# Kernel tuning notes

Hardware: AMD Instinct MI355X
Metric: run time of the kernel (lower is better)

## Reference

```python
import jax, jax.numpy as jnp
import numpy as np

FEW, BATCH, D, STEPS = 128, 4096, 512, 4


def setup_inputs() -> dict:
    key = jax.random.key(0)
    ks = jax.random.split(key, 6)
    H = 2 * D  # LSTMCell hidden size
    return {
        "support": jax.random.normal(ks[0], (FEW, D), jnp.float32),
        "query": jax.random.normal(ks[1], (BATCH, D), jnp.float32),
        "W_ih": jax.random.normal(ks[2], (4 * H, D), jnp.float32) * (1.0 / np.sqrt(H)),
        "W_hh": jax.random.normal(ks[3], (4 * H, H), jnp.float32) * (1.0 / np.sqrt(H)),
        "b_ih": jax.random.normal(ks[4], (4 * H,), jnp.float32) * 0.01,
        "b_hh": jax.random.normal(ks[5], (4 * H,), jnp.float32) * 0.01,
        "process_step": STEPS,
    }


def reference(support, query, W_ih, W_hh, b_ih, b_hh, process_step):
    # support: (few, d); query: (batch, d); LSTMCell hidden = 2d.
    d = query.shape[1]
    batch = query.shape[0]
    h_r = jnp.zeros((batch, 2 * d), query.dtype)
    c = jnp.zeros((batch, 2 * d), query.dtype)
    h = query
    for _ in range(process_step):
        # PyTorch LSTMCell: gates ordered (i, f, g, o)
        gates = query @ W_ih.T + b_ih + h_r @ W_hh.T + b_hh  # (batch, 8d)
        i, f, g, o = jnp.split(gates, 4, axis=1)
        c = jax.nn.sigmoid(f) * c + jax.nn.sigmoid(i) * jnp.tanh(g)
        h_r_ = jax.nn.sigmoid(o) * jnp.tanh(c)  # (batch, 2d)
        h = query + h_r_[:, :d]  # (batch, d)
        attn = jax.nn.softmax(h @ support.T, axis=1)  # (batch, few)
        r = attn @ support  # (batch, d)
        h_r = jnp.concatenate([h, r], axis=1)  # (batch, 2d)
    return h
```

## Files before the change

### kernel.cpp

```cpp
#include <hip/hip_runtime.h>

#define BATCH 4096
#define DDIM  512
#define FEWN  128
#define LDA1  640
#define GATEN 2048
#define CDIM  512

typedef unsigned short ushort_t;
typedef __attribute__((ext_vector_type(8))) short bf16x8;
typedef __attribute__((ext_vector_type(4))) float f32x4;

__device__ inline ushort_t f2bf(float f) {
  unsigned u = __float_as_uint(f);
  unsigned r = (u + 0x7FFFu + ((u >> 16) & 1u)) >> 16;
  return (ushort_t)r;
}
__device__ inline float bf2f(ushort_t h) { return __uint_as_float((unsigned)h << 16); }
__device__ inline float bf2f_u(unsigned h16) { return __uint_as_float(h16 << 16); }

__device__ inline float sigmoidf(float x) { return 1.f / (1.f + __expf(-x)); }
__device__ inline float tanh_fast(float x) {
  float ax = fabsf(x);
  float t = __expf(-2.f * ax);
  float r = (1.f - t) / (1.f + t);
  return copysignf(r, x);
}

__device__ inline int orig_row(int colp) {
  return ((colp >> 4) & 3) * 1024 + ((colp >> 6) << 4) + (colp & 15);
}

__device__ inline void async_copy16(ushort_t* lds, const ushort_t* g) {
  __builtin_amdgcn_global_load_lds(
      (const __attribute__((address_space(1))) unsigned int*)g,
      (__attribute__((address_space(3))) unsigned int*)lds, 16, 0, 0);
}

#define XCD_SWZ()                                                            \
  int bx = blockIdx.x, by = blockIdx.y;                                      \
  {                                                                          \
    const int gx = gridDim.x;                                                \
    const int id = by * gx + bx;                                             \
    if ((gx & 7) == 0) {                                                     \
      const int cpx = gx >> 3;                                               \
      const int x = id & 7, s = id >> 3;                                     \
      bx = x * cpx + (s % cpx);                                              \
      by = s / cpx;                                                          \
    } else {                                                                 \
      const int nwg = gx * gridDim.y;                                        \
      const int qq = nwg >> 3, rr = nwg & 7;                                 \
      const int x = id & 7, s = id >> 3;                                     \
      const int nid = (x < rr ? x * (qq + 1) : rr * (qq + 1) + (x - rr) * qq) + s; \
      bx = nid % gx; by = nid / gx;                                          \
    }                                                                        \
  }

#define STAGE8(dA, dB, kk)                                                   \
    async_copy16(dA,              gA0 + (kk));                               \
    async_copy16(dA + 512,        gA0 + (size_t)16 * lda + (kk));            \
    async_copy16(dA + 4096,       gA0 + (kk) + 32);                          \
    async_copy16(dA + 4096 + 512, gA0 + (size_t)16 * lda + (kk) + 32);       \
    async_copy16(dB,              gB0 + (kk));                               \
    async_copy16(dB + 512,        gB0 + (size_t)16 * ldb + (kk));            \
    async_copy16(dB + 4096,       gB0 + (kk) + 32);                          \
    async_copy16(dB + 4096 + 512, gB0 + (size_t)16 * ldb + (kk) + 32);

#define KLOOP_DBUF()                                                         \
  const int nIter = K >> 6;                                                  \
  { STAGE8(sA, sB, 0) }                                                      \
  if (nIter > 1) { STAGE8(sA + 8192, sB + 8192, 64) }                        \
  for (int kt = 0; kt < nIter; ++kt) {                                       \
    if (kt + 1 < nIter) asm volatile("s_waitcnt vmcnt(8)" ::: "memory");     \
    else                asm volatile("s_waitcnt vmcnt(0)" ::: "memory");     \
    __builtin_amdgcn_s_barrier();                                            \
    const int cur = (kt & 1) * 8192;                                         \
    _Pragma("unroll")                                                        \
    for (int h = 0; h < 2; ++h) {                                            \
      bf16x8 af[4], bfr[4];                                                  \
      _Pragma("unroll")                                                      \
      for (int mi = 0; mi < 4; ++mi)                                         \
        af[mi] = *(const bf16x8*)&lA[cur + h * 4096 + (wr * 64 + mi * 16 + lr) * 32 + kg * 8]; \
      _Pragma("unroll")                                                      \
      for (int ni = 0; ni < 4; ++ni)                                         \
        bfr[ni] = *(const bf16x8*)&lB[cur + h * 4096 + (wc * 64 + ni * 16 + lr) * 32 + kg * 8]; \
      _Pragma("unroll")                                                      \
      for (int mi = 0; mi < 4; ++mi)                                         \
        _Pragma("unroll")                                                    \
        for (int ni = 0; ni < 4; ++ni)                                       \
          acc[mi][ni] = __builtin_amdgcn_mfma_f32_16x16x32_bf16(af[mi], bfr[ni], acc[mi][ni], 0, 0, 0); \
    }                                                                        \
    __builtin_amdgcn_s_barrier();                                            \
    if (kt + 2 < nIter) {                                                    \
      const int k2 = (kt + 2) << 6;                                          \
      STAGE8(sA + cur, sB + cur, k2)                                         \
    }                                                                        \
  }

#define GEMM_PROLOG()                                                        \
  __shared__ __align__(16) ushort_t lA[2 * 8192];                            \
  __shared__ __align__(16) ushort_t lB[2 * 8192];                            \
  const int tid = threadIdx.x;                                               \
  const int wid = tid >> 6, lane = tid & 63;                                 \
  const int wr = wid >> 1, wc = wid & 1;                                     \
  XCD_SWZ()                                                                  \
  const int m0 = by * 128, n0 = bx * 128;                                    \
  const int lr = lane & 15, kg = lane >> 4;                                  \
  f32x4 acc[4][4] = {};                                                      \
  const int srow = lane >> 2;                                                \
  const int scol = (lane & 3) * 8;                                           \
  const ushort_t* gA0 = A + (size_t)(m0 + wid * 32 + srow) * lda + scol;     \
  const ushort_t* gB0 = B + (size_t)(n0 + wid * 32 + srow) * ldb + scol;     \
  ushort_t* sA = &lA[wid * 1024];                                            \
  ushort_t* sB = &lB[wid * 1024];                                            \
  KLOOP_DBUF()

__launch_bounds__(256)
__global__ void gemm_wide(const ushort_t* __restrict__ A, const ushort_t* __restrict__ B,
                          ushort_t* __restrict__ gbase, ushort_t* __restrict__ c,
                          ushort_t* __restrict__ A1out, ushort_t* __restrict__ A2out,
                          const float* __restrict__ b1, const float* __restrict__ b2,
                          int K, int lda, int ldb) {
  GEMM_PROLOG()
  if (n0 < 2048) {
    const int jj = ((n0 + wc * 64) >> 6) * 16 + lr;
    const float bi0 = b1[jj]        + b2[jj];
    const float bi2 = b1[2048 + jj] + b2[2048 + jj];
    const float bi3 = b1[3072 + jj] + b2[3072 + jj];
#pragma unroll
    for (int mi = 0; mi < 4; ++mi) {
#pragma unroll
      for (int r = 0; r < 4; ++r) {
        const int row = m0 + wr * 64 + mi * 16 + kg * 4 + r;
        const float si = sigmoidf(acc[mi][0][r] + bi0);
        const float tg = tanh_fast(acc[mi][2][r] + bi2);
        const float so = sigmoidf(acc[mi][3][r] + bi3);
        const float cn = si * tg;
        c[(size_t)row * CDIM + jj] = f2bf(cn);
        const float hr = so * tanh_fast(cn);
        const ushort_t hi = f2bf(hr);
        const ushort_t lo = f2bf(hr - bf2f(hi));
        A1out[(size_t)row * LDA1 + jj] = hi;
        A2out[(size_t)row * DDIM + jj] = lo;
      }
    }
  } else {
    const int jj = ((n0 - 2048 + wc * 64) >> 6) * 16 + lr;
    const float bi0 = b1[jj]        + b2[jj];
    const float bi1 = b1[1024 + jj] + b2[1024 + jj];
    const float bi2 = b1[2048 + jj] + b2[2048 + jj];
    const float bi3 = b1[3072 + jj] + b2[3072 + jj];
#pragma unroll
    for (int mi = 0; mi < 4; ++mi)
#pragma unroll
      for (int r = 0; r < 4; ++r) {
        const int row = m0 + wr * 64 + mi * 16 + kg * 4 + r;
        uint2 p;
        p.x = (unsigned)f2bf(acc[mi][0][r] + bi0) | ((unsigned)f2bf(acc[mi][1][r] + bi1) << 16);
        p.y = (unsigned)f2bf(acc[mi][2][r] + bi2) | ((unsigned)f2bf(acc[mi][3][r] + bi3) << 16);
        *(uint2*)&gbase[(size_t)row * GATEN + jj * 4] = p;
      }
  }
}

template<int MODE>
__launch_bounds__(256)
__global__ void gemm_fused(const ushort_t* __restrict__ A, const ushort_t* __restrict__ B,
                           const ushort_t* __restrict__ base, ushort_t* __restrict__ c,
                           ushort_t* __restrict__ A1out, ushort_t* __restrict__ A2out,
                           const float* __restrict__ query, float* __restrict__ out,
                           int K, int lda, int ldb) {
  GEMM_PROLOG()
  const int jj = ((n0 + wc * 64) >> 6) * 16 + lr;
#pragma unroll
  for (int mi = 0; mi < 4; ++mi) {
#pragma unroll
    for (int r = 0; r < 4; ++r) {
      const int row = m0 + wr * 64 + mi * 16 + kg * 4 + r;
      const uint2 p = *(const uint2*)&base[(size_t)row * GATEN + jj * 4];
      const float g0 = bf2f_u(p.x & 0xFFFFu) + acc[mi][0][r];
      const float g1 = bf2f_u(p.x >> 16)     + acc[mi][1][r];
      const float g2 = bf2f_u(p.y & 0xFFFFu) + acc[mi][2][r];
      const float g3 = bf2f_u(p.y >> 16)     + acc[mi][3][r];
      const float si = sigmoidf(g0);
      const float sf = sigmoidf(g1);
      const float tg = tanh_fast(g2);
      const float so = sigmoidf(g3);
      const size_t ci = (size_t)row * CDIM + jj;
      const float cn = sf * bf2f(c[ci]) + si * tg;
      if (MODE != 2) c[ci] = f2bf(cn);
      const float hr = so * tanh_fast(cn);
      if (MODE == 2) {
        out[(size_t)row * DDIM + jj] = query[(size_t)row * DDIM + jj] + hr;
      } else {
        const ushort_t hi = f2bf(hr);
        const ushort_t lo = f2bf(hr - bf2f(hi));
        A1out[(size_t)row * LDA1 + jj] = hi;
        A2out[(size_t)row * DDIM + jj] = lo;
      }
    }
  }
}

__launch_bounds__(256)
__global__ void gemm_splitk6(const ushort_t* __restrict__ A1, const ushort_t* __restrict__ A2,
                             int lda1, int lda2,
                             const ushort_t* __restrict__ Bc, float* __restrict__ Cf) {
  __shared__ __align__(16) ushort_t lA[2 * 8192];
  __shared__ __align__(16) ushort_t lB[2 * 8192];
  const int tid = threadIdx.x;
  const int wid = tid >> 6, lane = tid & 63;
  const int wr = wid >> 1, wc = wid & 1;
  const int seg = blockIdx.x >> 1;
  const int koff = (blockIdx.x & 1) * 256;
  const int m0 = blockIdx.y * 128;
  const int lr = lane & 15, kg = lane >> 4;
  f32x4 acc[4][4] = {};
  const int srow = lane >> 2;
  const int scol = (lane & 3) * 8;
  const ushort_t* A = (seg == 1) ? A2 : A1;
  const int lda = (seg == 1) ? lda2 : lda1;
  const int ldb = 1536;
  const ushort_t* gA0 = A + (size_t)(m0 + wid * 32 + srow) * lda + koff + scol;
  const ushort_t* gB0 = Bc + (size_t)(wid * 32 + srow) * 1536 + seg * 512 + koff + scol;
  ushort_t* sA = &lA[wid * 1024];
  ushort_t* sB = &lB[wid * 1024];
  const int K = 256;
  KLOOP_DBUF()
#pragma unroll
  for (int mi = 0; mi < 4; ++mi)
#pragma unroll
    for (int ni = 0; ni < 4; ++ni)
#pragma unroll
      for (int r = 0; r < 4; ++r) {
        const int row = m0 + wr * 64 + mi * 16 + kg * 4 + r;
        const int col = wc * 64 + ni * 16 + lr;
        atomicAdd(&Cf[(size_t)row * FEWN + col], acc[mi][ni][r]);
      }
}

template<int EPI>
__launch_bounds__(256)
__global__ void gemm_bt(const ushort_t* __restrict__ A, const ushort_t* __restrict__ B,
                        float* __restrict__ Cf, ushort_t* __restrict__ Cb,
                        int K, int lda, int ldb, int ldc) {
  GEMM_PROLOG()
#pragma unroll
  for (int mi = 0; mi < 4; ++mi)
#pragma unroll
    for (int ni = 0; ni < 4; ++ni)
#pragma unroll
      for (int r = 0; r < 4; ++r) {
        const int row = m0 + wr * 64 + mi * 16 + kg * 4 + r;
        const int col = n0 + wc * 64 + ni * 16 + lr;
        const float v = acc[mi][ni][r];
        const size_t o = (size_t)row * ldc + col;
        if (EPI == 2) Cb[o] = f2bf(v);
        else          Cf[o] = v;
      }
}

__global__ void broadcast3(float* __restrict__ lg) {
  const size_t LOFS = (size_t)BATCH * FEWN;
  const int i = blockIdx.x * 256 + threadIdx.x;
  const float4 v = ((const float4*)lg)[i];
  ((float4*)(lg + LOFS))[i] = v;
  ((float4*)(lg + 2 * LOFS))[i] = v;
}

__global__ void softmax_kernel(const float* __restrict__ logits, ushort_t* __restrict__ A1) {
  const int row = blockIdx.x * 4 + (threadIdx.x >> 6);
  const int lane = threadIdx.x & 63;
  const float* L = logits + (size_t)row * FEWN;
  const float x0 = L[lane], x1 = L[lane + 64];
  float m = fmaxf(x0, x1);
#pragma unroll
  for (int s = 32; s > 0; s >>= 1) m = fmaxf(m, __shfl_xor(m, s));
  const float e0 = __expf(x0 - m), e1 = __expf(x1 - m);
  float sum = e0 + e1;
#pragma unroll
  for (int s = 32; s > 0; s >>= 1) sum += __shfl_xor(sum, s);
  const float inv = 1.f / sum;
  A1[(size_t)row * LDA1 + 512 + lane]      = f2bf(e0 * inv);
  A1[(size_t)row * LDA1 + 512 + 64 + lane] = f2bf(e1 * inv);
}

__global__ void build_wcomb(const float* __restrict__ Wih, const float* __restrict__ Whh,
                            ushort_t* __restrict__ out) {
  const int idx = blockIdx.x * 256 + threadIdx.x;
  const int r = idx >> 9, cc = idx & 511;
  ushort_t v;
  if (r < 2048) {
    v = f2bf(Wih[(size_t)orig_row(r) * 512 + cc]);
  } else {
    const int og = orig_row(r - 2048);
    v = f2bf(Wih[(size_t)og * 512 + cc] + Whh[(size_t)og * 1024 + cc]);
  }
  out[idx] = v;
}

__global__ void build_whh_both(const float* __restrict__ W, ushort_t* __restrict__ B2,
                               ushort_t* __restrict__ whhRP) {
  const int idx = blockIdx.x * 256 + threadIdx.x;
  const int r = idx >> 10, k = idx & 1023;
  const ushort_t v = f2bf(W[(size_t)orig_row(r) * 1024 + k]);
  if (k < 512) B2[(size_t)r * LDA1 + k] = v;
  else         whhRP[(size_t)r * 512 + (k - 512)] = v;
}

__global__ void build_qcat(const float* __restrict__ q, ushort_t* __restrict__ out) {
  const int idx = blockIdx.x * 256 + threadIdx.x;
  const int b = idx >> 9, cc = idx & 511;
  const float v = q[idx];
  const ushort_t hi = f2bf(v);
  const ushort_t lo = f2bf(v - bf2f(hi));
  const size_t ro = (size_t)b * 1536;
  out[ro + cc] = hi;
  out[ro + 512 + cc] = lo;
  out[ro + 1024 + cc] = hi;
}

__global__ void build_bcat(const float* __restrict__ s, ushort_t* __restrict__ out) {
  const int idx = blockIdx.x * 256 + threadIdx.x;
  const int n = idx >> 9, cc = idx & 511;
  const float v = s[idx];
  const ushort_t hi = f2bf(v);
  const ushort_t lo = f2bf(v - bf2f(hi));
  const size_t ro = (size_t)n * 1536;
  out[ro + cc] = hi;
  out[ro + 512 + cc] = hi;
  out[ro + 1024 + cc] = lo;
}

extern "C" void kernel_launch(void* const* d_in, const int* in_sizes, int n_in,
                              void* d_out, int out_size, void* d_ws, size_t ws_size,
                              hipStream_t stream) {
  const float* support = (const float*)d_in[0];
  const float* query   = (const float*)d_in[1];
  const float* W_ih    = (const float*)d_in[2];
  const float* W_hh    = (const float*)d_in[3];
  const float* b_ih    = (const float*)d_in[4];
  const float* b_hh    = (const float*)d_in[5];
  float* out = (float*)d_out;

  char* ws = (char*)d_ws;
  size_t off = 0;
  auto alloc = [&](size_t bytes) { char* p = ws + off; off += (bytes + 255) & ~255ull; return p; };
  ushort_t* gates_baseP = (ushort_t*)alloc((size_t)BATCH * GATEN * 2);
  ushort_t* cbuf        = (ushort_t*)alloc((size_t)BATCH * CDIM * 2);
  ushort_t* A1a         = (ushort_t*)alloc((size_t)BATCH * LDA1 * 2);
  ushort_t* A1b         = (ushort_t*)alloc((size_t)BATCH * LDA1 * 2);
  ushort_t* A2a         = (ushort_t*)alloc((size_t)BATCH * DDIM * 2);
  ushort_t* A2b         = (ushort_t*)alloc((size_t)BATCH * DDIM * 2);
  ushort_t* Q_cat       = (ushort_t*)alloc((size_t)BATCH * 1536 * 2);
  ushort_t* wcomb       = (ushort_t*)alloc((size_t)4096 * 512 * 2);
  ushort_t* B2          = (ushort_t*)alloc((size_t)GATEN * LDA1 * 2);
  ushort_t* whhRP       = (ushort_t*)alloc((size_t)GATEN * 512 * 2);
  ushort_t* B_cat       = (ushort_t*)alloc((size_t)FEWN * 1536 * 2);
  float*    logits3     = (float*)   alloc((size_t)3 * BATCH * FEWN * 4);

  const size_t LOFS = (size_t)BATCH * FEWN;
  const dim3 blk(256);

  build_wcomb<<<4096 * 512 / 256, blk, 0, stream>>>(W_ih, W_hh, wcomb);
  build_whh_both<<<GATEN * 1024 / 256, blk, 0, stream>>>(W_hh, B2, whhRP);
  build_qcat<<<BATCH * 512 / 256, blk, 0, stream>>>(query, Q_cat);
  build_bcat<<<FEWN * 512 / 256, blk, 0, stream>>>(support, B_cat);

  hipMemsetAsync(logits3, 0, LOFS * 4, stream);
  gemm_splitk6<<<dim3(6, 32), blk, 0, stream>>>(Q_cat, Q_cat + 512, 1536, 1536,
                                                B_cat, logits3);
  broadcast3<<<(int)(LOFS / 4 / 256), blk, 0, stream>>>(logits3);

  gemm_bt<2><<<dim3(1, 16), blk, 0, stream>>>(whhRP, B_cat, nullptr, B2 + 512,
                                              512, 512, 1536, LDA1);

  gemm_wide<<<dim3(32, 32), blk, 0, stream>>>(
      Q_cat, wcomb, gates_baseP, cbuf, A1a, A2a, b_ih, b_hh, 512, 1536, 512);

  auto attn_phase = [&](int s, ushort_t* A1, ushort_t* A2) {
    float* lg = logits3 + (size_t)s * LOFS;
    gemm_splitk6<<<dim3(6, 32), blk, 0, stream>>>(A1, A2, LDA1, DDIM, B_cat, lg);
    softmax_kernel<<<BATCH / 4, blk, 0, stream>>>(lg, A1);
  };

  attn_phase(0, A1a, A2a);

  gemm_fused<1><<<dim3(16, 32), blk, 0, stream>>>(
      A1a, B2, gates_baseP, cbuf, A1b, A2b, nullptr, nullptr, 640, LDA1, LDA1);
  attn_phase(1, A1b, A2b);

  gemm_fused<1><<<dim3(16, 32), blk, 0, stream>>>(
      A1b, B2, gates_baseP, cbuf, A1a, A2a, nullptr, nullptr, 640, LDA1, LDA1);
  attn_phase(2, A1a, A2a);

  gemm_fused<2><<<dim3(16, 32), blk, 0, stream>>>(
      A1a, B2, gates_baseP, cbuf, nullptr, nullptr, query, out, 640, LDA1, LDA1);
}
```

Baseline: 197.2 us.

## Fuse softmax into split-K attention GEMM via last-block counter; merge setup kernels

New measurement: 287.7 us. 1.46x slower.

```diff
diff --git a/kernel.cpp b/kernel.cpp
--- a/kernel.cpp
+++ b/kernel.cpp
@@ -202,10 +202,13 @@
   }
 }
 
+template<bool DOSM>
 __launch_bounds__(256)
 __global__ void gemm_splitk6(const ushort_t* __restrict__ A1, const ushort_t* __restrict__ A2,
                              int lda1, int lda2,
-                             const ushort_t* __restrict__ Bc, float* __restrict__ Cf) {
+                             const ushort_t* __restrict__ Bc, float* __restrict__ Cf,
+                             const float* __restrict__ baseL, ushort_t* __restrict__ A1att,
+                             unsigned* __restrict__ counter) {
   __shared__ __align__(16) ushort_t lA[2 * 8192];
   __shared__ __align__(16) ushort_t lB[2 * 8192];
   const int tid = threadIdx.x;
@@ -237,6 +240,36 @@
         const int col = wc * 64 + ni * 16 + lr;
         atomicAdd(&Cf[(size_t)row * FEWN + col], acc[mi][ni][r]);
       }
+  if (DOSM) {
+    __threadfence();
+    __syncthreads();
+    if (tid == 0) {
+      const unsigned old = __hip_atomic_fetch_add(counter + blockIdx.y, 1u,
+                                                  __ATOMIC_ACQ_REL, __HIP_MEMORY_SCOPE_AGENT);
+      ((int*)lA)[0] = (old == 5) ? 1 : 0;
+    }
+    __syncthreads();
+    if (((int*)lA)[0]) {
+      for (int i = 0; i < 32; ++i) {
+        const int row = m0 + wid * 32 + i;
+        const size_t ro = (size_t)row * FEWN;
+        float x0 = __hip_atomic_load(&Cf[ro + lane], __ATOMIC_RELAXED,
+                                     __HIP_MEMORY_SCOPE_AGENT) + baseL[ro + lane];
+        float x1 = __hip_atomic_load(&Cf[ro + 64 + lane], __ATOMIC_RELAXED,
+                                     __HIP_MEMORY_SCOPE_AGENT) + baseL[ro + 64 + lane];
+        float mm = fmaxf(x0, x1);
+#pragma unroll
+        for (int sd = 32; sd > 0; sd >>= 1) mm = fmaxf(mm, __shfl_xor(mm, sd));
+        const float e0 = __expf(x0 - mm), e1 = __expf(x1 - mm);
+        float sum = e0 + e1;
+#pragma unroll
+        for (int sd = 32; sd > 0; sd >>= 1) sum += __shfl_xor(sum, sd);
+        const float inv = 1.f / sum;
+        A1att[(size_t)row * LDA1 + 512 + lane]      = f2bf(e0 * inv);
+        A1att[(size_t)row * LDA1 + 512 + 64 + lane] = f2bf(e1 * inv);
+      }
+    }
+  }
 }
 
 template<int EPI>
@@ -260,76 +293,51 @@
       }
 }
 
-__global__ void broadcast3(float* __restrict__ lg) {
-  const size_t LOFS = (size_t)BATCH * FEWN;
-  const int i = blockIdx.x * 256 + threadIdx.x;
-  const float4 v = ((const float4*)lg)[i];
-  ((float4*)(lg + LOFS))[i] = v;
-  ((float4*)(lg + 2 * LOFS))[i] = v;
-}
-
-__global__ void softmax_kernel(const float* __restrict__ logits, ushort_t* __restrict__ A1) {
-  const int row = blockIdx.x * 4 + (threadIdx.x >> 6);
-  const int lane = threadIdx.x & 63;
-  const float* L = logits + (size_t)row * FEWN;
-  const float x0 = L[lane], x1 = L[lane + 64];
-  float m = fmaxf(x0, x1);
-#pragma unroll
-  for (int s = 32; s > 0; s >>= 1) m = fmaxf(m, __shfl_xor(m, s));
-  const float e0 = __expf(x0 - m), e1 = __expf(x1 - m);
-  float sum = e0 + e1;
-#pragma unroll
-  for (int s = 32; s > 0; s >>= 1) sum += __shfl_xor(sum, s);
-  const float inv = 1.f / sum;
-  A1[(size_t)row * LDA1 + 512 + lane]      = f2bf(e0 * inv);
-  A1[(size_t)row * LDA1 + 512 + 64 + lane] = f2bf(e1 * inv);
-}
-
-__global__ void build_wcomb(const float* __restrict__ Wih, const float* __restrict__ Whh,
-                            ushort_t* __restrict__ out) {
-  const int idx = blockIdx.x * 256 + threadIdx.x;
-  const int r = idx >> 9, cc = idx & 511;
-  ushort_t v;
-  if (r < 2048) {
-    v = f2bf(Wih[(size_t)orig_row(r) * 512 + cc]);
+__global__ void setup_all(const float* __restrict__ Wih, const float* __restrict__ Whh,
+                          const float* __restrict__ q, const float* __restrict__ s,
+                          ushort_t* __restrict__ wcomb, ushort_t* __restrict__ B2,
+                          ushort_t* __restrict__ whhRP, ushort_t* __restrict__ Q_cat,
+                          ushort_t* __restrict__ B_cat) {
+  const int b = blockIdx.x;
+  const int tid = threadIdx.x;
+  if (b < 8192) {
+    const int idx = b * 256 + tid;
+    const int r = idx >> 9, cc = idx & 511;
+    ushort_t v;
+    if (r < 2048) {
+      v = f2bf(Wih[(size_t)orig_row(r) * 512 + cc]);
+    } else {
+      const int og = orig_row(r - 2048);
+      v = f2bf(Wih[(size_t)og * 512 + cc] + Whh[(size_t)og * 1024 + cc]);
+    }
+    wcomb[idx] = v;
+  } else if (b < 16384) {
+    const int idx = (b - 8192) * 256 + tid;
+    const int r = idx >> 10, k = idx & 1023;
+    const ushort_t v = f2bf(Whh[(size_t)orig_row(r) * 1024 + k]);
+    if (k < 512) B2[(size_t)r * LDA1 + k] = v;
+    else         whhRP[(size_t)r * 512 + (k - 512)] = v;
+  } else if (b < 24576) {
+    const int idx = (b - 16384) * 256 + tid;
+    const int bb = idx >> 9, cc = idx & 511;
+    const float v = q[idx];
+    const ushort_t hi = f2bf(v);
+    const ushort_t lo = f2bf(v - bf2f(hi));
+    const size_t ro = (size_t)bb * 1536;
+    Q_cat[ro + cc] = hi;
+    Q_cat[ro + 512 + cc] = lo;
+    Q_cat[ro + 1024 + cc] = hi;
   } else {
-    const int og = orig_row(r - 2048);
-    v = f2bf(Wih[(size_t)og * 512 + cc] + Whh[(size_t)og * 1024 + cc]);
-  }
-  out[idx] = v;
-}
-
-__global__ void build_whh_both(const float* __restrict__ W, ushort_t* __restrict__ B2,
-                               ushort_t* __restrict__ whhRP) {
-  const int idx = blockIdx.x * 256 + threadIdx.x;
-  const int r = idx >> 10, k = idx & 1023;
-  const ushort_t v = f2bf(W[(size_t)orig_row(r) * 1024 + k]);
-  if (k < 512) B2[(size_t)r * LDA1 + k] = v;
-  else         whhRP[(size_t)r * 512 + (k - 512)] = v;
-}
-
-__global__ void build_qcat(const float* __restrict__ q, ushort_t* __restrict__ out) {
-  const int idx = blockIdx.x * 256 + threadIdx.x;
-  const int b = idx >> 9, cc = idx & 511;
-  const float v = q[idx];
-  const ushort_t hi = f2bf(v);
-  const ushort_t lo = f2bf(v - bf2f(hi));
-  const size_t ro = (size_t)b * 1536;
-  out[ro + cc] = hi;
-  out[ro + 512 + cc] = lo;
-  out[ro + 1024 + cc] = hi;
-}
-
-__global__ void build_bcat(const float* __restrict__ s, ushort_t* __restrict__ out) {
-  const int idx = blockIdx.x * 256 + threadIdx.x;
-  const int n = idx >> 9, cc = idx & 511;
-  const float v = s[idx];
-  const ushort_t hi = f2bf(v);
-  const ushort_t lo = f2bf(v - bf2f(hi));
-  const size_t ro = (size_t)n * 1536;
-  out[ro + cc] = hi;
-  out[ro + 512 + cc] = hi;
-  out[ro + 1024 + cc] = lo;
+    const int idx = (b - 24576) * 256 + tid;
+    const int n = idx >> 9, cc = idx & 511;
+    const float v = s[idx];
+    const ushort_t hi = f2bf(v);
+    const ushort_t lo = f2bf(v - bf2f(hi));
+    const size_t ro = (size_t)n * 1536;
+    B_cat[ro + cc] = hi;
+    B_cat[ro + 512 + cc] = hi;
+    B_cat[ro + 1024 + cc] = lo;
+  }
 }
 
 extern "C" void kernel_launch(void* const* d_in, const int* in_sizes, int n_in,
@@ -357,20 +365,20 @@
   ushort_t* B2          = (ushort_t*)alloc((size_t)GATEN * LDA1 * 2);
   ushort_t* whhRP       = (ushort_t*)alloc((size_t)GATEN * 512 * 2);
   ushort_t* B_cat       = (ushort_t*)alloc((size_t)FEWN * 1536 * 2);
-  float*    logits3     = (float*)   alloc((size_t)3 * BATCH * FEWN * 4);
-
   const size_t LOFS = (size_t)BATCH * FEWN;
+  float*    logits3     = (float*)   alloc(3 * LOFS * 4);
+  float*    lgBase      = (float*)   alloc(LOFS * 4);
+  unsigned* counters    = (unsigned*)alloc(3 * 32 * 4);
+  const size_t zbytes = 3 * LOFS * 4 + LOFS * 4 + 512;
+
   const dim3 blk(256);
 
-  build_wcomb<<<4096 * 512 / 256, blk, 0, stream>>>(W_ih, W_hh, wcomb);
-  build_whh_both<<<GATEN * 1024 / 256, blk, 0, stream>>>(W_hh, B2, whhRP);
-  build_qcat<<<BATCH * 512 / 256, blk, 0, stream>>>(query, Q_cat);
-  build_bcat<<<FEWN * 512 / 256, blk, 0, stream>>>(support, B_cat);
-
-  hipMemsetAsync(logits3, 0, LOFS * 4, stream);
-  gemm_splitk6<<<dim3(6, 32), blk, 0, stream>>>(Q_cat, Q_cat + 512, 1536, 1536,
-                                                B_cat, logits3);
-  broadcast3<<<(int)(LOFS / 4 / 256), blk, 0, stream>>>(logits3);
+  setup_all<<<24832, blk, 0, stream>>>(W_ih, W_hh, query, support,
+                                       wcomb, B2, whhRP, Q_cat, B_cat);
+  hipMemsetAsync(logits3, 0, zbytes, stream);
+
+  gemm_splitk6<false><<<dim3(6, 32), blk, 0, stream>>>(
+      Q_cat, Q_cat + 512, 1536, 1536, B_cat, lgBase, nullptr, nullptr, nullptr);
 
   gemm_bt<2><<<dim3(1, 16), blk, 0, stream>>>(whhRP, B_cat, nullptr, B2 + 512,
                                               512, 512, 1536, LDA1);
@@ -378,21 +386,18 @@
   gemm_wide<<<dim3(32, 32), blk, 0, stream>>>(
       Q_cat, wcomb, gates_baseP, cbuf, A1a, A2a, b_ih, b_hh, 512, 1536, 512);
 
-  auto attn_phase = [&](int s, ushort_t* A1, ushort_t* A2) {
-    float* lg = logits3 + (size_t)s * LOFS;
-    gemm_splitk6<<<dim3(6, 32), blk, 0, stream>>>(A1, A2, LDA1, DDIM, B_cat, lg);
-    softmax_kernel<<<BATCH / 4, blk, 0, stream>>>(lg, A1);
-  };
-
-  attn_phase(0, A1a, A2a);
+  gemm_splitk6<true><<<dim3(6, 32), blk, 0, stream>>>(
+      A1a, A2a, LDA1, DDIM, B_cat, logits3, lgBase, A1a, counters);
 
   gemm_fused<1><<<dim3(16, 32), blk, 0, stream>>>(
       A1a, B2, gates_baseP, cbuf, A1b, A2b, nullptr, nullptr, 640, LDA1, LDA1);
-  attn_phase(1, A1b, A2b);
+  gemm_splitk6<true><<<dim3(6, 32), blk, 0, stream>>>(
+      A1b, A2b, LDA1, DDIM, B_cat, logits3 + LOFS, lgBase, A1b, counters + 32);
 
   gemm_fused<1><<<dim3(16, 32), blk, 0, stream>>>(
       A1b, B2, gates_baseP, cbuf, A1a, A2a, nullptr, nullptr, 640, LDA1, LDA1);
-  attn_phase(2, A1a, A2a);
+  gemm_splitk6<true><<<dim3(6, 32), blk, 0, stream>>>(
+      A1a, A2a, LDA1, DDIM, B_cat, logits3 + 2 * LOFS, lgBase, A1a, counters + 64);
 
   gemm_fused<2><<<dim3(16, 32), blk, 0, stream>>>(
       A1a, B2, gates_baseP, cbuf, nullptr, nullptr, query, out, 640, LDA1, LDA1);
```
